# Optimization experiments

Hardware: AMD Instinct MI355X
Metric: run time of the kernel (lower is better)

Reference implementation:

```python
import jax, jax.numpy as jnp
import numpy as np

EPS = 1e-15  # matches torch_geometric dense pooling EPS


def gcn_conv(x, src, dst, w, W, b, n):
    # GCNConv(normalize=False): linear first, then weighted scatter-add src->dst, then bias
    h = x @ W
    msg = w[:, None] * h[src]  # [E, out]
    return jax.ops.segment_sum(msg, dst, num_segments=n) + b


def setup_inputs() -> dict:
    key = jax.random.key(0)
    ks = jax.random.split(key, 8)
    N, E, d, k = 12288, 393216, 256, 16
    x = jax.random.normal(ks[0], (N, d), dtype=jnp.float32)
    edge_index = jax.random.randint(ks[1], (2, E), 0, N, dtype=jnp.int32)
    edge_weight = jax.random.uniform(ks[2], (E,), dtype=jnp.float32)
    sc = 1.0 / np.sqrt(d).astype(np.float32)
    W1 = jax.random.normal(ks[3], (d, d), dtype=jnp.float32) * sc
    b1 = jnp.zeros((d,), jnp.float32)
    W2 = jax.random.normal(ks[4], (d, d), dtype=jnp.float32) * sc
    b2 = jnp.zeros((d,), jnp.float32)
    Wm = jax.random.normal(ks[5], (d, k), dtype=jnp.float32) * sc
    bm = jnp.zeros((k,), jnp.float32)
    return dict(x=x, edge_weight=edge_weight, W1=W1, b1=b1, W2=W2, b2=b2,
                Wm=Wm, bm=bm, edge_index=edge_index)


def reference(x, edge_weight, W1, b1, W2, b2, Wm, bm, edge_index):
    src, dst = edge_index[0], edge_index[1]
    n = x.shape[0]
    # message-passing stack: GCNConv -> ReLU -> GCNConv -> ReLU
    h = jax.nn.relu(gcn_conv(x, src, dst, edge_weight, W1, b1, n))
    h = jax.nn.relu(gcn_conv(h, src, dst, edge_weight, W2, b2, n))
    # cluster MLP (single Linear, Identity activations)
    s_logits = h @ Wm + bm  # [N, k]
    # to_dense_adj(edge_index, edge_attr=edge_weight): dense [N, N]
    adj = jnp.zeros((n, n), x.dtype).at[src, dst].add(edge_weight)
    # just_balance_pool (batch of 1)
    s = jax.nn.softmax(s_logits, axis=-1)  # [N, k]
    out = s.T @ h              # pooled features (unused by module output)
    out_adj = s.T @ adj @ s    # pooled adjacency (unused by module output)
    gram = s.T @ s             # [k, k]
    k = s.shape[-1]
    b_loss = -jnp.trace(jnp.sqrt(gram + EPS)) / jnp.sqrt(jnp.float32(n * k))
    return s, b_loss
```

## Files before the change

kernel.cpp:

```cpp
#include <hip/hip_runtime.h>
#include <hip/hip_bf16.h>
#include <hip/hip_fp16.h>

#define D 256
#define KCL 16
#define EPS 1e-15f
#define PAD 128

typedef __attribute__((ext_vector_type(8))) short short8;
typedef __attribute__((ext_vector_type(8))) _Float16 half8;
typedef __attribute__((ext_vector_type(4))) float f32x4;

__global__ __launch_bounds__(256) void setup_k(const float* __restrict__ W1,
                                               const float* __restrict__ W2,
                                               __half* __restrict__ Wt1,
                                               __half* __restrict__ Wt2,
                                               const int* __restrict__ src,
                                               const int* __restrict__ dst,
                                               const float* __restrict__ ew,
                                               int* __restrict__ deg,
                                               int2* __restrict__ edges, int E) {
    int b = blockIdx.x;
    if (b < 512) {
        const float* W = (b < 256) ? W1 : W2;
        __half* T = (b < 256) ? Wt1 : Wt2;
        int c = b & 255;
        int k = threadIdx.x;
        T[(size_t)c * D + k] = __float2half(W[(size_t)k * D + c]);
    } else {
        int e = (b - 512) * 256 + threadIdx.x;
        if (e < E) {
            int d = dst[e];
            int slot = atomicAdd(&deg[d], 1);
            if (slot < PAD)
                edges[(size_t)d * PAD + slot] = make_int2(src[e], __float_as_int(ew[e]));
        }
    }
}

__device__ __forceinline__ short8 ld8h(const float* p) {
    float4 v0 = *(const float4*)p;
    float4 v1 = *(const float4*)(p + 4);
    float vv[8] = {v0.x, v0.y, v0.z, v0.w, v1.x, v1.y, v1.z, v1.w};
    short8 o;
#pragma unroll
    for (int j = 0; j < 8; ++j) {
        _Float16 h = (_Float16)vv[j];
        o[j] = __builtin_bit_cast(short, h);
    }
    return o;
}
__device__ __forceinline__ short8 ld8h(const __half* p) {
    return *(const short8*)p;
}

template<typename T>
__global__ __launch_bounds__(256) void gemm_k(const T* __restrict__ A,
                                              const __half* __restrict__ Bt,
                                              __half* __restrict__ C) {
    __shared__ short Ah[64][40];
    int tid = threadIdx.x;
    int lane = tid & 63, w = tid >> 6;
    int bm = blockIdx.x * 64, bn = blockIdx.y * 64;
    f32x4 acc[4];
#pragma unroll
    for (int i = 0; i < 4; ++i) acc[i] = (f32x4){0.f, 0.f, 0.f, 0.f};

    int r  = tid >> 2;
    int cc = (tid & 3) * 8;
    int ar = w * 16 + (lane & 15);
    int kq = (lane >> 4) * 8;

    for (int kk = 0; kk < D; kk += 32) {
        short8 a8 = ld8h(&A[(size_t)(bm + r) * D + kk + cc]);
        __syncthreads();
        *(short8*)&Ah[r][cc] = a8;
        __syncthreads();

        half8 av = __builtin_bit_cast(half8, *(const short8*)&Ah[ar][kq]);
#pragma unroll
        for (int nf = 0; nf < 4; ++nf) {
            int col = bn + nf * 16 + (lane & 15);
            half8 bv = __builtin_bit_cast(half8,
                        *(const short8*)&Bt[(size_t)col * D + kk + kq]);
            acc[nf] = __builtin_amdgcn_mfma_f32_16x16x32_f16(av, bv, acc[nf], 0, 0, 0);
        }
    }
    int rbase = bm + w * 16 + (lane >> 4) * 4;
    int cb = bn + (lane & 15);
#pragma unroll
    for (int nf = 0; nf < 4; ++nf)
#pragma unroll
        for (int rr = 0; rr < 4; ++rr)
            C[(size_t)(rbase + rr) * D + cb + nf * 16] = __float2half(acc[nf][rr]);
}

__global__ __launch_bounds__(128) void spmm_k(const __half* __restrict__ h,
                                              const int2* __restrict__ edges,
                                              const int* __restrict__ deg,
                                              const float* __restrict__ bias,
                                              __half* __restrict__ out) {
    int node = blockIdx.x;
    int t = threadIdx.x;
    int n = min(deg[node], PAD);
    __shared__ int2 se[PAD];
    if (t < n) se[t] = edges[(size_t)node * PAD + t];
    __syncthreads();
    const __half2* h2 = (const __half2*)h;
    float acc0 = 0.f, acc1 = 0.f;
    int i = 0;
    for (; i + 4 <= n; i += 4) {
        int2 e0 = se[i], e1 = se[i + 1], e2 = se[i + 2], e3 = se[i + 3];
        float2 a0 = __half22float2(h2[(size_t)e0.x * (D / 2) + t]);
        float2 a1 = __half22float2(h2[(size_t)e1.x * (D / 2) + t]);
        float2 a2 = __half22float2(h2[(size_t)e2.x * (D / 2) + t]);
        float2 a3 = __half22float2(h2[(size_t)e3.x * (D / 2) + t]);
        float w0 = __int_as_float(e0.y), w1 = __int_as_float(e1.y);
        float w2 = __int_as_float(e2.y), w3 = __int_as_float(e3.y);
        acc0 = fmaf(w0, a0.x, acc0); acc1 = fmaf(w0, a0.y, acc1);
        acc0 = fmaf(w1, a1.x, acc0); acc1 = fmaf(w1, a1.y, acc1);
        acc0 = fmaf(w2, a2.x, acc0); acc1 = fmaf(w2, a2.y, acc1);
        acc0 = fmaf(w3, a3.x, acc0); acc1 = fmaf(w3, a3.y, acc1);
    }
    for (; i < n; ++i) {
        int2 e = se[i];
        float2 a = __half22float2(h2[(size_t)e.x * (D / 2) + t]);
        float wv = __int_as_float(e.y);
        acc0 = fmaf(wv, a.x, acc0); acc1 = fmaf(wv, a.y, acc1);
    }
    float2 bv = *(const float2*)&bias[2 * t];
    float f0 = fmaxf(acc0 + bv.x, 0.f), f1 = fmaxf(acc1 + bv.y, 0.f);
    ((__half2*)out)[(size_t)node * (D / 2) + t] = __float22half2_rn(make_float2(f0, f1));
}

__global__ __launch_bounds__(128) void spmm_cluster_k(const __half* __restrict__ h,
                                                      const int2* __restrict__ edges,
                                                      const int* __restrict__ deg,
                                                      const float* __restrict__ bias,
                                                      const float* __restrict__ Wm,
                                                      const float* __restrict__ bmv,
                                                      float* __restrict__ s_out) {
    int node = blockIdx.x;
    int t = threadIdx.x;
    int n = min(deg[node], PAD);
    __shared__ int2 se[PAD];
    if (t < n) se[t] = edges[(size_t)node * PAD + t];
    __syncthreads();
    const __half2* h2 = (const __half2*)h;
    float acc0 = 0.f, acc1 = 0.f;
    int i = 0;
    for (; i + 4 <= n; i += 4) {
        int2 e0 = se[i], e1 = se[i + 1], e2 = se[i + 2], e3 = se[i + 3];
        float2 a0 = __half22float2(h2[(size_t)e0.x * (D / 2) + t]);
        float2 a1 = __half22float2(h2[(size_t)e1.x * (D / 2) + t]);
        float2 a2 = __half22float2(h2[(size_t)e2.x * (D / 2) + t]);
        float2 a3 = __half22float2(h2[(size_t)e3.x * (D / 2) + t]);
        float w0 = __int_as_float(e0.y), w1 = __int_as_float(e1.y);
        float w2 = __int_as_float(e2.y), w3 = __int_as_float(e3.y);
        acc0 = fmaf(w0, a0.x, acc0); acc1 = fmaf(w0, a0.y, acc1);
        acc0 = fmaf(w1, a1.x, acc0); acc1 = fmaf(w1, a1.y, acc1);
        acc0 = fmaf(w2, a2.x, acc0); acc1 = fmaf(w2, a2.y, acc1);
        acc0 = fmaf(w3, a3.x, acc0); acc1 = fmaf(w3, a3.y, acc1);
    }
    for (; i < n; ++i) {
        int2 e = se[i];
        float2 a = __half22float2(h2[(size_t)e.x * (D / 2) + t]);
        float wv = __int_as_float(e.y);
        acc0 = fmaf(wv, a.x, acc0); acc1 = fmaf(wv, a.y, acc1);
    }
    float2 bv = *(const float2*)&bias[2 * t];
    float f0 = fmaxf(acc0 + bv.x, 0.f), f1 = fmaxf(acc1 + bv.y, 0.f);

    float pl[KCL];
    const float4* w0 = (const float4*)&Wm[(size_t)(2 * t) * KCL];
    const float4* w1 = (const float4*)&Wm[(size_t)(2 * t + 1) * KCL];
#pragma unroll
    for (int q = 0; q < 4; ++q) {
        float4 a = w0[q], b = w1[q];
        pl[q * 4 + 0] = f0 * a.x + f1 * b.x;
        pl[q * 4 + 1] = f0 * a.y + f1 * b.y;
        pl[q * 4 + 2] = f0 * a.z + f1 * b.z;
        pl[q * 4 + 3] = f0 * a.w + f1 * b.w;
    }
#pragma unroll
    for (int off = 32; off; off >>= 1)
#pragma unroll
        for (int j = 0; j < KCL; ++j) pl[j] += __shfl_xor(pl[j], off, 64);
    __shared__ float xw[2][KCL];
    int wv = t >> 6, ln = t & 63;
    if (ln == 0) {
#pragma unroll
        for (int j = 0; j < KCL; ++j) xw[wv][j] = pl[j];
    }
    __syncthreads();
    if (t == 0) {
        float p[KCL];
        float mx = -1e30f;
#pragma unroll
        for (int j = 0; j < KCL; ++j) {
            p[j] = xw[0][j] + xw[1][j] + bmv[j];
            mx = fmaxf(mx, p[j]);
        }
        float sum = 0.f;
#pragma unroll
        for (int j = 0; j < KCL; ++j) { p[j] = __expf(p[j] - mx); sum += p[j]; }
        float inv = 1.f / sum;
        float* so = &s_out[(size_t)node * KCL];
#pragma unroll
        for (int q = 0; q < 4; ++q)
            *(float4*)&so[q * 4] = make_float4(p[q*4+0] * inv, p[q*4+1] * inv,
                                               p[q*4+2] * inv, p[q*4+3] * inv);
    }
}

__global__ __launch_bounds__(256) void sqloss_k(const float* __restrict__ s,
                                                float* __restrict__ diag,
                                                int* __restrict__ done,
                                                float* __restrict__ loss_out, int N) {
    int tid = threadIdx.x;
    int j = tid & 15;
    int g = tid >> 4;
    int total = N * KCL;
    float acc = 0.f;
    for (int idx = blockIdx.x * 256 + tid; idx < total; idx += gridDim.x * 256) {
        float v = s[idx];
        acc = fmaf(v, v, acc);
    }
    __shared__ float red[16][17];
    red[g][j] = acc;
    __syncthreads();
    if (g == 0) {
        float a = red[0][j];
#pragma unroll
        for (int gg = 1; gg < 16; ++gg) a += red[gg][j];
        atomicAdd(&diag[j], a);
    }
    __threadfence();
    __shared__ int lastFlag;
    if (tid == 0) {
        int old = atomicAdd(done, 1);
        lastFlag = (old == (int)gridDim.x - 1);
    }
    __syncthreads();
    if (lastFlag && tid == 0) {
        __threadfence();
        float sum = 0.f;
#pragma unroll
        for (int jj = 0; jj < KCL; ++jj) {
            float v = atomicAdd(&diag[jj], 0.f);
            sum += sqrtf(v + EPS);
        }
        loss_out[0] = -sum / sqrtf((float)N * (float)KCL);
    }
}

extern "C" void kernel_launch(void* const* d_in, const int* in_sizes, int n_in,
                              void* d_out, int out_size, void* d_ws, size_t ws_size,
                              hipStream_t stream) {
    const float* x  = (const float*)d_in[0];
    const float* ew = (const float*)d_in[1];
    const float* W1 = (const float*)d_in[2];
    const float* b1 = (const float*)d_in[3];
    const float* W2 = (const float*)d_in[4];
    const float* b2 = (const float*)d_in[5];
    const float* Wm = (const float*)d_in[6];
    const float* bm = (const float*)d_in[7];
    const int*   ei = (const int*)d_in[8];

    const int N = in_sizes[0] / D;
    const int E = in_sizes[1];
    const int* src = ei;
    const int* dst = ei + E;

    float* out = (float*)d_out;

    char* ws = (char*)d_ws;
    __half* G    = (__half*)ws;       ws += (size_t)N * D * 2;
    __half* H1   = (__half*)ws;       ws += (size_t)N * D * 2;
    int*   deg   = (int*)ws;          ws += (size_t)N * 4;
    float* diag  = (float*)ws;        ws += 64;
    int*   done  = (int*)ws;          ws += 16;
    int2*  edges = (int2*)ws;         ws += (size_t)N * PAD * 8;
    __half* Wt1  = (__half*)ws;       ws += (size_t)D * D * 2;
    __half* Wt2  = (__half*)ws;       ws += (size_t)D * D * 2;

    hipMemsetAsync(deg, 0, (size_t)N * 4 + 80, stream);
    int gE = (E + 255) / 256;
    setup_k<<<512 + gE, 256, 0, stream>>>(W1, W2, Wt1, Wt2,
                                          src, dst, ew, deg, edges, E);

    dim3 ggrid(N / 64, 4);
    gemm_k<float><<<ggrid, 256, 0, stream>>>(x, Wt1, G);
    spmm_k<<<N, 128, 0, stream>>>(G, edges, deg, b1, H1);
    gemm_k<__half><<<ggrid, 256, 0, stream>>>(H1, Wt2, G);
    spmm_cluster_k<<<N, 128, 0, stream>>>(G, edges, deg, b2, Wm, bm, out);
    sqloss_k<<<64, 256, 0, stream>>>(out, diag, done, out + (size_t)N * KCL, N);
}
```

Measured before the change: 214.4 us.

## Map one wavefront per node in SpMM kernels with 8-byte gathers

```diff
diff --git a/kernel.cpp b/kernel.cpp
--- a/kernel.cpp
+++ b/kernel.cpp
@@ -95,121 +95,124 @@
             C[(size_t)(rbase + rr) * D + cb + nf * 16] = __float2half(acc[nf][rr]);
 }
 
-__global__ __launch_bounds__(128) void spmm_k(const __half* __restrict__ h,
+__device__ __forceinline__ void spmm_wave(const __half* __restrict__ h,
+                                          const int2* __restrict__ edges,
+                                          int node, int n, int lane,
+                                          int2* se, float f[4]) {
+    if (lane < n) se[lane] = edges[(size_t)node * PAD + lane];
+    if (lane + 64 < n) se[lane + 64] = edges[(size_t)node * PAD + lane + 64];
+    float a0 = 0.f, a1 = 0.f, a2 = 0.f, a3 = 0.f;
+    int i = 0;
+    for (; i + 4 <= n; i += 4) {
+        int2 e0 = se[i], e1 = se[i + 1], e2 = se[i + 2], e3 = se[i + 3];
+        float2 r0 = ((const float2*)(h + (size_t)e0.x * D))[lane];
+        float2 r1 = ((const float2*)(h + (size_t)e1.x * D))[lane];
+        float2 r2 = ((const float2*)(h + (size_t)e2.x * D))[lane];
+        float2 r3 = ((const float2*)(h + (size_t)e3.x * D))[lane];
+        float w0 = __int_as_float(e0.y), w1 = __int_as_float(e1.y);
+        float w2 = __int_as_float(e2.y), w3 = __int_as_float(e3.y);
+        float2 p, q;
+        p = __half22float2(__builtin_bit_cast(__half2, r0.x));
+        q = __half22float2(__builtin_bit_cast(__half2, r0.y));
+        a0 = fmaf(w0, p.x, a0); a1 = fmaf(w0, p.y, a1);
+        a2 = fmaf(w0, q.x, a2); a3 = fmaf(w0, q.y, a3);
+        p = __half22float2(__builtin_bit_cast(__half2, r1.x));
+        q = __half22float2(__builtin_bit_cast(__half2, r1.y));
+        a0 = fmaf(w1, p.x, a0); a1 = fmaf(w1, p.y, a1);
+        a2 = fmaf(w1, q.x, a2); a3 = fmaf(w1, q.y, a3);
+        p = __half22float2(__builtin_bit_cast(__half2, r2.x));
+        q = __half22float2(__builtin_bit_cast(__half2, r2.y));
+        a0 = fmaf(w2, p.x, a0); a1 = fmaf(w2, p.y, a1);
+        a2 = fmaf(w2, q.x, a2); a3 = fmaf(w2, q.y, a3);
+        p = __half22float2(__builtin_bit_cast(__half2, r3.x));
+        q = __half22float2(__builtin_bit_cast(__half2, r3.y));
+        a0 = fmaf(w3, p.x, a0); a1 = fmaf(w3, p.y, a1);
+        a2 = fmaf(w3, q.x, a2); a3 = fmaf(w3, q.y, a3);
+    }
+    for (; i < n; ++i) {
+        int2 e = se[i];
+        float2 r = ((const float2*)(h + (size_t)e.x * D))[lane];
+        float wv = __int_as_float(e.y);
+        float2 p = __half22float2(__builtin_bit_cast(__half2, r.x));
+        float2 q = __half22float2(__builtin_bit_cast(__half2, r.y));
+        a0 = fmaf(wv, p.x, a0); a1 = fmaf(wv, p.y, a1);
+        a2 = fmaf(wv, q.x, a2); a3 = fmaf(wv, q.y, a3);
+    }
+    f[0] = a0; f[1] = a1; f[2] = a2; f[3] = a3;
+}
+
+__global__ __launch_bounds__(256) void spmm_k(const __half* __restrict__ h,
                                               const int2* __restrict__ edges,
                                               const int* __restrict__ deg,
                                               const float* __restrict__ bias,
                                               __half* __restrict__ out) {
-    int node = blockIdx.x;
-    int t = threadIdx.x;
+    __shared__ int2 se[4][PAD];
+    int tid = threadIdx.x;
+    int wv = tid >> 6, lane = tid & 63;
+    int node = blockIdx.x * 4 + wv;
     int n = min(deg[node], PAD);
-    __shared__ int2 se[PAD];
-    if (t < n) se[t] = edges[(size_t)node * PAD + t];
-    __syncthreads();
-    const __half2* h2 = (const __half2*)h;
-    float acc0 = 0.f, acc1 = 0.f;
-    int i = 0;
-    for (; i + 4 <= n; i += 4) {
-        int2 e0 = se[i], e1 = se[i + 1], e2 = se[i + 2], e3 = se[i + 3];
-        float2 a0 = __half22float2(h2[(size_t)e0.x * (D / 2) + t]);
-        float2 a1 = __half22float2(h2[(size_t)e1.x * (D / 2) + t]);
-        float2 a2 = __half22float2(h2[(size_t)e2.x * (D / 2) + t]);
-        float2 a3 = __half22float2(h2[(size_t)e3.x * (D / 2) + t]);
-        float w0 = __int_as_float(e0.y), w1 = __int_as_float(e1.y);
-        float w2 = __int_as_float(e2.y), w3 = __int_as_float(e3.y);
-        acc0 = fmaf(w0, a0.x, acc0); acc1 = fmaf(w0, a0.y, acc1);
-        acc0 = fmaf(w1, a1.x, acc0); acc1 = fmaf(w1, a1.y, acc1);
-        acc0 = fmaf(w2, a2.x, acc0); acc1 = fmaf(w2, a2.y, acc1);
-        acc0 = fmaf(w3, a3.x, acc0); acc1 = fmaf(w3, a3.y, acc1);
-    }
-    for (; i < n; ++i) {
-        int2 e = se[i];
-        float2 a = __half22float2(h2[(size_t)e.x * (D / 2) + t]);
-        float wv = __int_as_float(e.y);
-        acc0 = fmaf(wv, a.x, acc0); acc1 = fmaf(wv, a.y, acc1);
-    }
-    float2 bv = *(const float2*)&bias[2 * t];
-    float f0 = fmaxf(acc0 + bv.x, 0.f), f1 = fmaxf(acc1 + bv.y, 0.f);
-    ((__half2*)out)[(size_t)node * (D / 2) + t] = __float22half2_rn(make_float2(f0, f1));
-}
-
-__global__ __launch_bounds__(128) void spmm_cluster_k(const __half* __restrict__ h,
+    float f[4];
+    spmm_wave(h, edges, node, n, lane, se[wv], f);
+    float4 bv = ((const float4*)bias)[lane];
+    __half2 o01 = __float22half2_rn(make_float2(fmaxf(f[0] + bv.x, 0.f),
+                                                fmaxf(f[1] + bv.y, 0.f)));
+    __half2 o23 = __float22half2_rn(make_float2(fmaxf(f[2] + bv.z, 0.f),
+                                                fmaxf(f[3] + bv.w, 0.f)));
+    ((float2*)(out + (size_t)node * D))[lane] =
+        make_float2(__builtin_bit_cast(float, o01), __builtin_bit_cast(float, o23));
+}
+
+__global__ __launch_bounds__(256) void spmm_cluster_k(const __half* __restrict__ h,
                                                       const int2* __restrict__ edges,
                                                       const int* __restrict__ deg,
                                                       const float* __restrict__ bias,
                                                       const float* __restrict__ Wm,
                                                       const float* __restrict__ bmv,
                                                       float* __restrict__ s_out) {
-    int node = blockIdx.x;
-    int t = threadIdx.x;
+    __shared__ int2 se[4][PAD];
+    int tid = threadIdx.x;
+    int wv = tid >> 6, lane = tid & 63;
+    int node = blockIdx.x * 4 + wv;
     int n = min(deg[node], PAD);
-    __shared__ int2 se[PAD];
-    if (t < n) se[t] = edges[(size_t)node * PAD + t];
-    __syncthreads();
-    const __half2* h2 = (const __half2*)h;
-    float acc0 = 0.f, acc1 = 0.f;
-    int i = 0;
-    for (; i + 4 <= n; i += 4) {
-        int2 e0 = se[i], e1 = se[i + 1], e2 = se[i + 2], e3 = se[i + 3];
-        float2 a0 = __half22float2(h2[(size_t)e0.x * (D / 2) + t]);
-        float2 a1 = __half22float2(h2[(size_t)e1.x * (D / 2) + t]);
-        float2 a2 = __half22float2(h2[(size_t)e2.x * (D / 2) + t]);
-        float2 a3 = __half22float2(h2[(size_t)e3.x * (D / 2) + t]);
-        float w0 = __int_as_float(e0.y), w1 = __int_as_float(e1.y);
-        float w2 = __int_as_float(e2.y), w3 = __int_as_float(e3.y);
-        acc0 = fmaf(w0, a0.x, acc0); acc1 = fmaf(w0, a0.y, acc1);
-        acc0 = fmaf(w1, a1.x, acc0); acc1 = fmaf(w1, a1.y, acc1);
-        acc0 = fmaf(w2, a2.x, acc0); acc1 = fmaf(w2, a2.y, acc1);
-        acc0 = fmaf(w3, a3.x, acc0); acc1 = fmaf(w3, a3.y, acc1);
-    }
-    for (; i < n; ++i) {
-        int2 e = se[i];
-        float2 a = __half22float2(h2[(size_t)e.x * (D / 2) + t]);
-        float wv = __int_as_float(e.y);
-        acc0 = fmaf(wv, a.x, acc0); acc1 = fmaf(wv, a.y, acc1);
-    }
-    float2 bv = *(const float2*)&bias[2 * t];
-    float f0 = fmaxf(acc0 + bv.x, 0.f), f1 = fmaxf(acc1 + bv.y, 0.f);
+    float f[4];
+    spmm_wave(h, edges, node, n, lane, se[wv], f);
+    float4 bv = ((const float4*)bias)[lane];
+    f[0] = fmaxf(f[0] + bv.x, 0.f); f[1] = fmaxf(f[1] + bv.y, 0.f);
+    f[2] = fmaxf(f[2] + bv.z, 0.f); f[3] = fmaxf(f[3] + bv.w, 0.f);
 
     float pl[KCL];
-    const float4* w0 = (const float4*)&Wm[(size_t)(2 * t) * KCL];
-    const float4* w1 = (const float4*)&Wm[(size_t)(2 * t + 1) * KCL];
-#pragma unroll
-    for (int q = 0; q < 4; ++q) {
-        float4 a = w0[q], b = w1[q];
-        pl[q * 4 + 0] = f0 * a.x + f1 * b.x;
-        pl[q * 4 + 1] = f0 * a.y + f1 * b.y;
-        pl[q * 4 + 2] = f0 * a.z + f1 * b.z;
-        pl[q * 4 + 3] = f0 * a.w + f1 * b.w;
+#pragma unroll
+    for (int j = 0; j < KCL; ++j) pl[j] = 0.f;
+#pragma unroll
+    for (int u = 0; u < 4; ++u) {
+        const float4* wr = (const float4*)&Wm[(size_t)(4 * lane + u) * KCL];
+        float fv = f[u];
+#pragma unroll
+        for (int q = 0; q < 4; ++q) {
+            float4 a = wr[q];
+            pl[q * 4 + 0] = fmaf(fv, a.x, pl[q * 4 + 0]);
+            pl[q * 4 + 1] = fmaf(fv, a.y, pl[q * 4 + 1]);
+            pl[q * 4 + 2] = fmaf(fv, a.z, pl[q * 4 + 2]);
+            pl[q * 4 + 3] = fmaf(fv, a.w, pl[q * 4 + 3]);
+        }
     }
 #pragma unroll
     for (int off = 32; off; off >>= 1)
 #pragma unroll
         for (int j = 0; j < KCL; ++j) pl[j] += __shfl_xor(pl[j], off, 64);
-    __shared__ float xw[2][KCL];
-    int wv = t >> 6, ln = t & 63;
-    if (ln == 0) {
-#pragma unroll
-        for (int j = 0; j < KCL; ++j) xw[wv][j] = pl[j];
-    }
-    __syncthreads();
-    if (t == 0) {
-        float p[KCL];
+    if (lane == 0) {
         float mx = -1e30f;
 #pragma unroll
-        for (int j = 0; j < KCL; ++j) {
-            p[j] = xw[0][j] + xw[1][j] + bmv[j];
-            mx = fmaxf(mx, p[j]);
-        }
+        for (int j = 0; j < KCL; ++j) { pl[j] += bmv[j]; mx = fmaxf(mx, pl[j]); }
         float sum = 0.f;
 #pragma unroll
-        for (int j = 0; j < KCL; ++j) { p[j] = __expf(p[j] - mx); sum += p[j]; }
+        for (int j = 0; j < KCL; ++j) { pl[j] = __expf(pl[j] - mx); sum += pl[j]; }
         float inv = 1.f / sum;
         float* so = &s_out[(size_t)node * KCL];
 #pragma unroll
         for (int q = 0; q < 4; ++q)
-            *(float4*)&so[q * 4] = make_float4(p[q*4+0] * inv, p[q*4+1] * inv,
-                                               p[q*4+2] * inv, p[q*4+3] * inv);
+            *(float4*)&so[q * 4] = make_float4(pl[q*4+0] * inv, pl[q*4+1] * inv,
+                                               pl[q*4+2] * inv, pl[q*4+3] * inv);
     }
 }
 
@@ -291,8 +294,8 @@
 
     dim3 ggrid(N / 64, 4);
     gemm_k<float><<<ggrid, 256, 0, stream>>>(x, Wt1, G);
-    spmm_k<<<N, 128, 0, stream>>>(G, edges, deg, b1, H1);
+    spmm_k<<<N / 4, 256, 0, stream>>>(G, edges, deg, b1, H1);
     gemm_k<__half><<<ggrid, 256, 0, stream>>>(H1, Wt2, G);
-    spmm_cluster_k<<<N, 128, 0, stream>>>(G, edges, deg, b2, Wm, bm, out);
+    spmm_cluster_k<<<N / 4, 256, 0, stream>>>(G, edges, deg, b2, Wm, bm, out);
     sqloss_k<<<64, 256, 0, stream>>>(out, diag, done, out + (size_t)N * KCL, N);
 }
```

After: 214.0 us. About the same (-0.2%).
